# Kernel optimization log

Measured on AMD Instinct MI355X. Metric: run time of the kernel, lower is better.

The kernel has to match this reference:

```python
import jax, jax.numpy as jnp
import numpy as np

T, F_IN, UNITS, N_CLASSES = 21, 126, 8, 27


def _run_lstm(seq, Wk, Wr, b):
    """Keras-style LSTM (gate order i,f,g,o). seq: (B,T,F) -> hs: (B,T,U)."""
    B = seq.shape[0]
    U = Wr.shape[0]
    # input projection for all timesteps at once: (B,T,4U)
    z_in = jnp.einsum('btf,fg->btg', seq, Wk) + b

    def step(carry, z_t):
        h, c = carry
        z = z_t + h @ Wr
        i, f, g, o = jnp.split(z, 4, axis=-1)
        i = jax.nn.sigmoid(i)
        f = jax.nn.sigmoid(f)
        g = jnp.tanh(g)
        o = jax.nn.sigmoid(o)
        c = f * c + i * g
        h = o * jnp.tanh(c)
        return (h, c), h

    h0 = jnp.zeros((B, U), seq.dtype)
    (_, _), hs = jax.lax.scan(step, (h0, h0), jnp.swapaxes(z_in, 0, 1))
    return jnp.swapaxes(hs, 0, 1)  # (B,T,U)


def setup_inputs() -> dict:
    key = jax.random.key(0)
    ks = jax.random.split(key, 6)
    B = 32768
    return {
        'x': jax.random.normal(ks[0], (B, T * F_IN), dtype=jnp.float32),
        'W1k': jax.random.normal(ks[1], (F_IN, 4 * UNITS), dtype=jnp.float32) * 0.1,
        'W1r': jax.random.normal(ks[2], (UNITS, 4 * UNITS), dtype=jnp.float32) * 0.1,
        'b1': jnp.zeros((4 * UNITS,), jnp.float32),
        'W2k': jax.random.normal(ks[3], (UNITS, 4 * UNITS), dtype=jnp.float32) * 0.1,
        'W2r': jax.random.normal(ks[4], (UNITS, 4 * UNITS), dtype=jnp.float32) * 0.1,
        'b2': jnp.zeros((4 * UNITS,), jnp.float32),
        'Wd': jax.random.normal(ks[5], (UNITS, N_CLASSES), dtype=jnp.float32) * 0.1,
        'bd': jnp.zeros((N_CLASSES,), jnp.float32),
    }


def reference(x, W1k, W1r, b1, W2k, W2r, b2, Wd, bd):
    B = x.shape[0]
    seq = x.reshape(B, T, F_IN)            # Reshape((21, 126))
    h1 = _run_lstm(seq, W1k, W1r, b1)      # LSTM(8, return_sequences=True)
    # dropout is identity at inference
    h2 = _run_lstm(h1, W2k, W2r, b2)[:, -1]  # LSTM(8) -> last step (B,8)
    return jax.nn.softmax(h2 @ Wd + bd)    # Dense(27, softmax)
```

## Files before the change

### kernel.cpp

```cpp
#include <hip/hip_runtime.h>


namespace {
constexpr int T_   = 21;
constexpr int FIN  = 126;
constexpr int U_   = 8;
constexpr int NC   = 27;
constexpr int BS   = 64;
constexpr int NTH  = 256;
constexpr int ROW  = T_ * FIN;
}

__device__ __forceinline__ float sigm(float x) {
  return __builtin_amdgcn_rcpf(1.0f + __expf(-x));
}
__device__ __forceinline__ float tanh_f(float x) {
  return 1.0f - 2.0f * __builtin_amdgcn_rcpf(1.0f + __expf(2.0f * x));
}

__global__ __launch_bounds__(NTH, 2) void lstm2_dense(
    const float* __restrict__ X,
    const float* __restrict__ W1k, const float* __restrict__ W1r,
    const float* __restrict__ b1,
    const float* __restrict__ W2k, const float* __restrict__ W2r,
    const float* __restrict__ b2,
    const float* __restrict__ Wd, const float* __restrict__ bd,
    float* __restrict__ out)
{
  __shared__ __align__(16) float xbuf[BS * FIN];
  __shared__ __align__(16) float zb1[4 * U_ * BS];
  __shared__ __align__(16) float zb2[4 * U_ * BS];

  const int tid = threadIdx.x;
  const int sl  = tid & 63;
  const int wv  = __builtin_amdgcn_readfirstlane(tid >> 6);
  const int blk = blockIdx.x;

  const float4* W1k4 = reinterpret_cast<const float4*>(W1k) + 2 * wv;
  const float4* W1r4 = reinterpret_cast<const float4*>(W1r) + 2 * wv;
  const float4* W2k4 = reinterpret_cast<const float4*>(W2k) + 2 * wv;
  const float4* W2r4 = reinterpret_cast<const float4*>(W2r) + 2 * wv;
  const float4  b1a = reinterpret_cast<const float4*>(b1)[2 * wv];
  const float4  b1b = reinterpret_cast<const float4*>(b1)[2 * wv + 1];
  const float4  b2a = reinterpret_cast<const float4*>(b2)[2 * wv];
  const float4  b2b = reinterpret_cast<const float4*>(b2)[2 * wv + 1];

  float c1[U_], h1[U_], c2[U_], h2[U_];
  #pragma unroll
  for (int u = 0; u < U_; ++u) { c1[u] = 0.f; h1[u] = 0.f; c2[u] = 0.f; h2[u] = 0.f; }

  const float* xbase = X + (size_t)blk * BS * ROW;

  for (int t = 0; t < T_; ++t) {
    #pragma unroll
    for (int k = 0; k < 16; ++k) {
      int j = tid + k * NTH;
      if (j < BS * 63) {
        int s = j / 63;
        int q = j - s * 63;
        float2 v = *reinterpret_cast<const float2*>(
            xbase + (size_t)s * ROW + t * FIN + 2 * q);
        *reinterpret_cast<float2*>(&xbuf[s * FIN + 2 * q]) = v;
      }
    }
    __syncthreads();

    float4 za = b1a, zb = b1b;
    {
      const float2* xr = reinterpret_cast<const float2*>(&xbuf[sl * FIN]);
      #pragma unroll 3
      for (int q = 0; q < 63; ++q) {
        float2 xv = xr[q];
        float4 wa0 = W1k4[(2 * q) * 8];
        float4 wb0 = W1k4[(2 * q) * 8 + 1];
        float4 wa1 = W1k4[(2 * q + 1) * 8];
        float4 wb1 = W1k4[(2 * q + 1) * 8 + 1];
        za.x += xv.x * wa0.x; za.y += xv.x * wa0.y; za.z += xv.x * wa0.z; za.w += xv.x * wa0.w;
        zb.x += xv.x * wb0.x; zb.y += xv.x * wb0.y; zb.z += xv.x * wb0.z; zb.w += xv.x * wb0.w;
        za.x += xv.y * wa1.x; za.y += xv.y * wa1.y; za.z += xv.y * wa1.z; za.w += xv.y * wa1.w;
        zb.x += xv.y * wb1.x; zb.y += xv.y * wb1.y; zb.z += xv.y * wb1.z; zb.w += xv.y * wb1.w;
      }
    }
    #pragma unroll
    for (int k = 0; k < U_; ++k) {
      float hv = h1[k];
      float4 wa = W1r4[k * 8];
      float4 wb = W1r4[k * 8 + 1];
      za.x += hv * wa.x; za.y += hv * wa.y; za.z += hv * wa.z; za.w += hv * wa.w;
      zb.x += hv * wb.x; zb.y += hv * wb.y; zb.z += hv * wb.z; zb.w += hv * wb.w;
    }
    {
      float* zp = &zb1[(8 * wv) * BS + sl];
      zp[0 * BS] = za.x; zp[1 * BS] = za.y; zp[2 * BS] = za.z; zp[3 * BS] = za.w;
      zp[4 * BS] = zb.x; zp[5 * BS] = zb.y; zp[6 * BS] = zb.z; zp[7 * BS] = zb.w;
    }
    __syncthreads();

    #pragma unroll
    for (int u = 0; u < U_; ++u) {
      float zi = zb1[u * BS + sl];
      float zf = zb1[(U_ + u) * BS + sl];
      float zg = zb1[(2 * U_ + u) * BS + sl];
      float zo = zb1[(3 * U_ + u) * BS + sl];
      float iv = sigm(zi), fv = sigm(zf), gv = tanh_f(zg), ov = sigm(zo);
      float cn = fv * c1[u] + iv * gv;
      c1[u] = cn;
      h1[u] = ov * tanh_f(cn);
    }

    za = b2a; zb = b2b;
    #pragma unroll
    for (int k = 0; k < U_; ++k) {
      float hv = h1[k];
      float4 wa = W2k4[k * 8];
      float4 wb = W2k4[k * 8 + 1];
      za.x += hv * wa.x; za.y += hv * wa.y; za.z += hv * wa.z; za.w += hv * wa.w;
      zb.x += hv * wb.x; zb.y += hv * wb.y; zb.z += hv * wb.z; zb.w += hv * wb.w;
    }
    #pragma unroll
    for (int k = 0; k < U_; ++k) {
      float hv = h2[k];
      float4 wa = W2r4[k * 8];
      float4 wb = W2r4[k * 8 + 1];
      za.x += hv * wa.x; za.y += hv * wa.y; za.z += hv * wa.z; za.w += hv * wa.w;
      zb.x += hv * wb.x; zb.y += hv * wb.y; zb.z += hv * wb.z; zb.w += hv * wb.w;
    }
    {
      float* zp = &zb2[(8 * wv) * BS + sl];
      zp[0 * BS] = za.x; zp[1 * BS] = za.y; zp[2 * BS] = za.z; zp[3 * BS] = za.w;
      zp[4 * BS] = zb.x; zp[5 * BS] = zb.y; zp[6 * BS] = zb.z; zp[7 * BS] = zb.w;
    }
    __syncthreads();

    #pragma unroll
    for (int u = 0; u < U_; ++u) {
      float zi = zb2[u * BS + sl];
      float zf = zb2[(U_ + u) * BS + sl];
      float zg = zb2[(2 * U_ + u) * BS + sl];
      float zo = zb2[(3 * U_ + u) * BS + sl];
      float iv = sigm(zi), fv = sigm(zf), gv = tanh_f(zg), ov = sigm(zo);
      float cn = fv * c2[u] + iv * gv;
      c2[u] = cn;
      h2[u] = ov * tanh_f(cn);
    }
  }

  float logits[NC];
  float m = -1e30f;
  #pragma unroll
  for (int c = 0; c < NC; ++c) {
    float acc = bd[c];
    #pragma unroll
    for (int k = 0; k < U_; ++k) acc += h2[k] * Wd[k * NC + c];
    logits[c] = acc;
    m = fmaxf(m, acc);
  }
  float ssum = 0.f;
  #pragma unroll
  for (int c = 0; c < NC; ++c) {
    float e = __expf(logits[c] - m);
    logits[c] = e;
    ssum += e;
  }
  float inv = 1.0f / ssum;
  if (wv == 0) {
    #pragma unroll
    for (int c = 0; c < NC; ++c) zb1[sl * NC + c] = logits[c] * inv;
  }
  __syncthreads();
  {
    float* oblk = out + (size_t)blk * BS * NC;
    #pragma unroll
    for (int k = 0; k < 7; ++k) {
      int j = tid + k * NTH;
      if (j < BS * NC) oblk[j] = zb1[j];
    }
  }
}

extern "C" void kernel_launch(void* const* d_in, const int* in_sizes, int n_in,
                              void* d_out, int out_size, void* d_ws, size_t ws_size,
                              hipStream_t stream) {
  const float* X   = (const float*)d_in[0];
  const float* W1k = (const float*)d_in[1];
  const float* W1r = (const float*)d_in[2];
  const float* b1  = (const float*)d_in[3];
  const float* W2k = (const float*)d_in[4];
  const float* W2r = (const float*)d_in[5];
  const float* b2  = (const float*)d_in[6];
  const float* Wd  = (const float*)d_in[7];
  const float* bd  = (const float*)d_in[8];
  float* out = (float*)d_out;

  const int B = in_sizes[0] / ROW;
  dim3 grid(B / BS), block(NTH);
  lstm2_dense<<<grid, block, 0, stream>>>(X, W1k, W1r, b1, W2k, W2r, b2,
                                          Wd, bd, out);
}
```

Baseline: 605.4 us.

## Split LSTM into parallel input-projection GEMM and per-wave recurrent kernel

Replaces the single fused kernel with two kernels. The first computes the layer-1 input projection for every timestep in parallel (grid over batch groups × time) and writes it to workspace. The second runs the recurrence with one wave per 64 sequences, keeping all 32 gates per thread in registers, so the shared-memory barriers disappear. This exposes more parallelism for the dominant GEMM and removes per-step syncs, at the cost of a global workspace round-trip, extra launches when the workspace is small, and uncoalesced X row reads in the GEMM.

```diff
diff --git a/kernel.cpp b/kernel.cpp
--- a/kernel.cpp
+++ b/kernel.cpp
@@ -2,13 +2,13 @@
 
 
 namespace {
-constexpr int T_   = 21;
-constexpr int FIN  = 126;
-constexpr int U_   = 8;
-constexpr int NC   = 27;
-constexpr int BS   = 64;
-constexpr int NTH  = 256;
-constexpr int ROW  = T_ * FIN;
+constexpr int T_  = 21;
+constexpr int FIN = 126;
+constexpr int U_  = 8;
+constexpr int NC  = 27;
+constexpr int ZC  = 4 * U_;
+constexpr int ROW = T_ * FIN;
+constexpr size_t ZGRP = (size_t)T_ * ZC * 64;
 }
 
 __device__ __forceinline__ float sigm(float x) {
@@ -18,164 +18,133 @@
   return 1.0f - 2.0f * __builtin_amdgcn_rcpf(1.0f + __expf(2.0f * x));
 }
 
-__global__ __launch_bounds__(NTH, 2) void lstm2_dense(
-    const float* __restrict__ X,
-    const float* __restrict__ W1k, const float* __restrict__ W1r,
-    const float* __restrict__ b1,
+__global__ __launch_bounds__(256) void zin_gemm(
+    const float* __restrict__ X, const float* __restrict__ W1k,
+    const float* __restrict__ b1, float* __restrict__ Z,
+    int g0, int g1)
+{
+  const int sl  = threadIdx.x & 63;
+  const int wv  = __builtin_amdgcn_readfirstlane(threadIdx.x >> 6);
+  const int grp = g0 + blockIdx.x * 4 + wv;
+  if (grp >= g1) return;
+  const int t = blockIdx.y;
+  const int b = grp * 64 + sl;
+
+  float acc[ZC];
+  #pragma unroll
+  for (int c = 0; c < ZC; ++c) acc[c] = b1[c];
+
+  const float2* xr = reinterpret_cast<const float2*>(X + (size_t)b * ROW + t * FIN);
+  #pragma unroll 3
+  for (int q = 0; q < 63; ++q) {
+    float2 xv = xr[q];
+    #pragma unroll
+    for (int c = 0; c < ZC; ++c) acc[c] = fmaf(xv.x, W1k[(2 * q) * ZC + c], acc[c]);
+    #pragma unroll
+    for (int c = 0; c < ZC; ++c) acc[c] = fmaf(xv.y, W1k[(2 * q + 1) * ZC + c], acc[c]);
+  }
+
+  float* zp = Z + (size_t)(grp - g0) * ZGRP + (size_t)t * ZC * 64 + sl;
+  #pragma unroll
+  for (int c = 0; c < ZC; ++c) zp[c * 64] = acc[c];
+}
+
+__global__ __launch_bounds__(64) void lstm_rec(
+    const float* __restrict__ Z,
+    const float* __restrict__ W1r,
     const float* __restrict__ W2k, const float* __restrict__ W2r,
     const float* __restrict__ b2,
     const float* __restrict__ Wd, const float* __restrict__ bd,
-    float* __restrict__ out)
+    float* __restrict__ out, int g0, int g1)
 {
-  __shared__ __align__(16) float xbuf[BS * FIN];
-  __shared__ __align__(16) float zb1[4 * U_ * BS];
-  __shared__ __align__(16) float zb2[4 * U_ * BS];
+  const int sl  = threadIdx.x & 63;
+  const int grp = g0 + blockIdx.x;
+  if (grp >= g1) return;
 
-  const int tid = threadIdx.x;
-  const int sl  = tid & 63;
-  const int wv  = __builtin_amdgcn_readfirstlane(tid >> 6);
-  const int blk = blockIdx.x;
+  const float* zb = Z + (size_t)(grp - g0) * ZGRP + sl;
 
-  const float4* W1k4 = reinterpret_cast<const float4*>(W1k) + 2 * wv;
-  const float4* W1r4 = reinterpret_cast<const float4*>(W1r) + 2 * wv;
-  const float4* W2k4 = reinterpret_cast<const float4*>(W2k) + 2 * wv;
-  const float4* W2r4 = reinterpret_cast<const float4*>(W2r) + 2 * wv;
-  const float4  b1a = reinterpret_cast<const float4*>(b1)[2 * wv];
-  const float4  b1b = reinterpret_cast<const float4*>(b1)[2 * wv + 1];
-  const float4  b2a = reinterpret_cast<const float4*>(b2)[2 * wv];
-  const float4  b2b = reinterpret_cast<const float4*>(b2)[2 * wv + 1];
+  float h1[U_], c1[U_], h2[U_], c2[U_];
+  #pragma unroll
+  for (int u = 0; u < U_; ++u) { h1[u] = 0.f; c1[u] = 0.f; h2[u] = 0.f; c2[u] = 0.f; }
 
-  float c1[U_], h1[U_], c2[U_], h2[U_];
+  float zc[ZC], zn[ZC];
   #pragma unroll
-  for (int u = 0; u < U_; ++u) { c1[u] = 0.f; h1[u] = 0.f; c2[u] = 0.f; h2[u] = 0.f; }
-
-  const float* xbase = X + (size_t)blk * BS * ROW;
+  for (int c = 0; c < ZC; ++c) zc[c] = zb[c * 64];
 
   for (int t = 0; t < T_; ++t) {
+    if (t + 1 < T_) {
+      const float* zt = zb + (size_t)(t + 1) * ZC * 64;
+      #pragma unroll
+      for (int c = 0; c < ZC; ++c) zn[c] = zt[c * 64];
+    }
+
+    float z1[ZC];
     #pragma unroll
-    for (int k = 0; k < 16; ++k) {
-      int j = tid + k * NTH;
-      if (j < BS * 63) {
-        int s = j / 63;
-        int q = j - s * 63;
-        float2 v = *reinterpret_cast<const float2*>(
-            xbase + (size_t)s * ROW + t * FIN + 2 * q);
-        *reinterpret_cast<float2*>(&xbuf[s * FIN + 2 * q]) = v;
-      }
-    }
-    __syncthreads();
-
-    float4 za = b1a, zb = b1b;
-    {
-      const float2* xr = reinterpret_cast<const float2*>(&xbuf[sl * FIN]);
-      #pragma unroll 3
-      for (int q = 0; q < 63; ++q) {
-        float2 xv = xr[q];
-        float4 wa0 = W1k4[(2 * q) * 8];
-        float4 wb0 = W1k4[(2 * q) * 8 + 1];
-        float4 wa1 = W1k4[(2 * q + 1) * 8];
-        float4 wb1 = W1k4[(2 * q + 1) * 8 + 1];
-        za.x += xv.x * wa0.x; za.y += xv.x * wa0.y; za.z += xv.x * wa0.z; za.w += xv.x * wa0.w;
-        zb.x += xv.x * wb0.x; zb.y += xv.x * wb0.y; zb.z += xv.x * wb0.z; zb.w += xv.x * wb0.w;
-        za.x += xv.y * wa1.x; za.y += xv.y * wa1.y; za.z += xv.y * wa1.z; za.w += xv.y * wa1.w;
-        zb.x += xv.y * wb1.x; zb.y += xv.y * wb1.y; zb.z += xv.y * wb1.z; zb.w += xv.y * wb1.w;
-      }
-    }
+    for (int c = 0; c < ZC; ++c) z1[c] = zc[c];
     #pragma unroll
     for (int k = 0; k < U_; ++k) {
       float hv = h1[k];
-      float4 wa = W1r4[k * 8];
-      float4 wb = W1r4[k * 8 + 1];
-      za.x += hv * wa.x; za.y += hv * wa.y; za.z += hv * wa.z; za.w += hv * wa.w;
-      zb.x += hv * wb.x; zb.y += hv * wb.y; zb.z += hv * wb.z; zb.w += hv * wb.w;
+      #pragma unroll
+      for (int c = 0; c < ZC; ++c) z1[c] = fmaf(hv, W1r[k * ZC + c], z1[c]);
     }
-    {
-      float* zp = &zb1[(8 * wv) * BS + sl];
-      zp[0 * BS] = za.x; zp[1 * BS] = za.y; zp[2 * BS] = za.z; zp[3 * BS] = za.w;
-      zp[4 * BS] = zb.x; zp[5 * BS] = zb.y; zp[6 * BS] = zb.z; zp[7 * BS] = zb.w;
-    }
-    __syncthreads();
-
     #pragma unroll
     for (int u = 0; u < U_; ++u) {
-      float zi = zb1[u * BS + sl];
-      float zf = zb1[(U_ + u) * BS + sl];
-      float zg = zb1[(2 * U_ + u) * BS + sl];
-      float zo = zb1[(3 * U_ + u) * BS + sl];
-      float iv = sigm(zi), fv = sigm(zf), gv = tanh_f(zg), ov = sigm(zo);
+      float iv = sigm(z1[u]), fv = sigm(z1[U_ + u]);
+      float gv = tanh_f(z1[2 * U_ + u]), ov = sigm(z1[3 * U_ + u]);
       float cn = fv * c1[u] + iv * gv;
       c1[u] = cn;
       h1[u] = ov * tanh_f(cn);
     }
 
-    za = b2a; zb = b2b;
+    float z2[ZC];
+    #pragma unroll
+    for (int c = 0; c < ZC; ++c) z2[c] = b2[c];
     #pragma unroll
     for (int k = 0; k < U_; ++k) {
       float hv = h1[k];
-      float4 wa = W2k4[k * 8];
-      float4 wb = W2k4[k * 8 + 1];
-      za.x += hv * wa.x; za.y += hv * wa.y; za.z += hv * wa.z; za.w += hv * wa.w;
-      zb.x += hv * wb.x; zb.y += hv * wb.y; zb.z += hv * wb.z; zb.w += hv * wb.w;
+      #pragma unroll
+      for (int c = 0; c < ZC; ++c) z2[c] = fmaf(hv, W2k[k * ZC + c], z2[c]);
     }
     #pragma unroll
     for (int k = 0; k < U_; ++k) {
       float hv = h2[k];
-      float4 wa = W2r4[k * 8];
-      float4 wb = W2r4[k * 8 + 1];
-      za.x += hv * wa.x; za.y += hv * wa.y; za.z += hv * wa.z; za.w += hv * wa.w;
-      zb.x += hv * wb.x; zb.y += hv * wb.y; zb.z += hv * wb.z; zb.w += hv * wb.w;
+      #pragma unroll
+      for (int c = 0; c < ZC; ++c) z2[c] = fmaf(hv, W2r[k * ZC + c], z2[c]);
     }
-    {
-      float* zp = &zb2[(8 * wv) * BS + sl];
-      zp[0 * BS] = za.x; zp[1 * BS] = za.y; zp[2 * BS] = za.z; zp[3 * BS] = za.w;
-      zp[4 * BS] = zb.x; zp[5 * BS] = zb.y; zp[6 * BS] = zb.z; zp[7 * BS] = zb.w;
-    }
-    __syncthreads();
-
     #pragma unroll
     for (int u = 0; u < U_; ++u) {
-      float zi = zb2[u * BS + sl];
-      float zf = zb2[(U_ + u) * BS + sl];
-      float zg = zb2[(2 * U_ + u) * BS + sl];
-      float zo = zb2[(3 * U_ + u) * BS + sl];
-      float iv = sigm(zi), fv = sigm(zf), gv = tanh_f(zg), ov = sigm(zo);
+      float iv = sigm(z2[u]), fv = sigm(z2[U_ + u]);
+      float gv = tanh_f(z2[2 * U_ + u]), ov = sigm(z2[3 * U_ + u]);
       float cn = fv * c2[u] + iv * gv;
       c2[u] = cn;
       h2[u] = ov * tanh_f(cn);
     }
+
+    #pragma unroll
+    for (int c = 0; c < ZC; ++c) zc[c] = zn[c];
   }
 
-  float logits[NC];
+  float lg[NC];
   float m = -1e30f;
   #pragma unroll
   for (int c = 0; c < NC; ++c) {
     float acc = bd[c];
     #pragma unroll
-    for (int k = 0; k < U_; ++k) acc += h2[k] * Wd[k * NC + c];
-    logits[c] = acc;
+    for (int k = 0; k < U_; ++k) acc = fmaf(h2[k], Wd[k * NC + c], acc);
+    lg[c] = acc;
     m = fmaxf(m, acc);
   }
   float ssum = 0.f;
   #pragma unroll
   for (int c = 0; c < NC; ++c) {
-    float e = __expf(logits[c] - m);
-    logits[c] = e;
+    float e = __expf(lg[c] - m);
+    lg[c] = e;
     ssum += e;
   }
   float inv = 1.0f / ssum;
-  if (wv == 0) {
-    #pragma unroll
-    for (int c = 0; c < NC; ++c) zb1[sl * NC + c] = logits[c] * inv;
-  }
-  __syncthreads();
-  {
-    float* oblk = out + (size_t)blk * BS * NC;
-    #pragma unroll
-    for (int k = 0; k < 7; ++k) {
-      int j = tid + k * NTH;
-      if (j < BS * NC) oblk[j] = zb1[j];
-    }
-  }
+  float* op = out + (size_t)(grp * 64 + sl) * NC;
+  #pragma unroll
+  for (int c = 0; c < NC; ++c) op[c] = lg[c] * inv;
 }
 
 extern "C" void kernel_launch(void* const* d_in, const int* in_sizes, int n_in,
@@ -191,9 +160,22 @@
   const float* Wd  = (const float*)d_in[7];
   const float* bd  = (const float*)d_in[8];
   float* out = (float*)d_out;
+  float* Z   = (float*)d_ws;
 
-  const int B = in_sizes[0] / ROW;
-  dim3 grid(B / BS), block(NTH);
-  lstm2_dense<<<grid, block, 0, stream>>>(X, W1k, W1r, b1, W2k, W2r, b2,
-                                          Wd, bd, out);
+  const int B    = in_sizes[0] / ROW;
+  const int ngrp = B / 64;
+
+  const size_t zgrp_bytes = ZGRP * sizeof(float);
+  int gpc = (int)((ws_size / zgrp_bytes));
+  if (gpc < 1) gpc = 1;
+  if (gpc > ngrp) gpc = ngrp;
+
+  for (int g0 = 0; g0 < ngrp; g0 += gpc) {
+    int g1 = g0 + gpc;
+    if (g1 > ngrp) g1 = ngrp;
+    int n = g1 - g0;
+    dim3 ggrid((n + 3) / 4, T_);
+    zin_gemm<<<ggrid, 256, 0, stream>>>(X, W1k, b1, Z, g0, g1);
+    lstm_rec<<<dim3(n), 64, 0, stream>>>(Z, W1r, W2k, W2r, b2, Wd, bd, out, g0, g1);
+  }
 }
```

Measured after the change: 695.7 us. +14.9%, slower.
